# Kernel tuning notes

Hardware: AMD Instinct MI355X
Metric: run time of the kernel (lower is better)

The kernel has to match this reference:

```python
import jax, jax.numpy as jnp
import numpy as np
from math import sqrt as msqrt

D_MODEL, D_FF, N_HEADS, D_K, D_V = 1024, 4096, 16, 64, 64
NEG = -1e9

def gelu_erf(x):
    return 0.5 * x * (1.0 + jax.lax.erf(x / msqrt(2.0)))

def layer_norm(x, g, b, eps=1e-5):
    mu = jnp.mean(x, axis=-1, keepdims=True)
    var = jnp.mean(jnp.square(x - mu), axis=-1, keepdims=True)
    return (x - mu) * jax.lax.rsqrt(var + eps) * g + b

def setup_inputs() -> dict:
    key = jax.random.key(0)
    ks = jax.random.split(key, 12)
    B, S = 2, 2048
    s = lambda fan_in: 1.0 / msqrt(fan_in)
    inp = {
        "x": jax.random.normal(ks[0], (B, S, D_MODEL), dtype=jnp.float32),
        "pad_mask": jnp.zeros((B, S, S), dtype=bool),
        "W_Q": jax.random.uniform(ks[1], (D_MODEL, N_HEADS * D_K), minval=-s(D_MODEL), maxval=s(D_MODEL)),
        "W_K": jax.random.uniform(ks[2], (D_MODEL, N_HEADS * D_K), minval=-s(D_MODEL), maxval=s(D_MODEL)),
        "W_V": jax.random.uniform(ks[3], (D_MODEL, N_HEADS * D_V), minval=-s(D_MODEL), maxval=s(D_MODEL)),
        "W_O": jax.random.uniform(ks[4], (N_HEADS * D_V, D_MODEL), minval=-s(N_HEADS * D_V), maxval=s(N_HEADS * D_V)),
        "fc1_w": jax.random.uniform(ks[5], (D_MODEL, D_FF), minval=-s(D_MODEL), maxval=s(D_MODEL)),
        "fc1_b": jax.random.uniform(ks[6], (D_FF,), minval=-s(D_MODEL), maxval=s(D_MODEL)),
        "fc2_w": jax.random.uniform(ks[7], (D_FF, D_MODEL), minval=-s(D_FF), maxval=s(D_FF)),
        "fc2_b": jax.random.uniform(ks[8], (D_MODEL,), minval=-s(D_FF), maxval=s(D_FF)),
        "ln1_g": jnp.ones((D_MODEL,), jnp.float32),
        "ln1_b": jnp.zeros((D_MODEL,), jnp.float32),
        "ln2_g": jnp.ones((D_MODEL,), jnp.float32),
        "ln2_b": jnp.zeros((D_MODEL,), jnp.float32),
    }
    return inp

def reference(x, pad_mask, W_Q, W_K, W_V, W_O, fc1_w, fc1_b, fc2_w, fc2_b,
              ln1_g, ln1_b, ln2_g, ln2_b):
    B, S, _ = x.shape
    # --- pre-norm MHA ---
    residual = x
    h = layer_norm(x, ln1_g, ln1_b)
    q = (h @ W_Q).reshape(B, S, N_HEADS, D_K).transpose(0, 2, 1, 3)  # [B,H,S,dk]
    k = (h @ W_K).reshape(B, S, N_HEADS, D_K).transpose(0, 2, 1, 3)
    v = (h @ W_V).reshape(B, S, N_HEADS, D_V).transpose(0, 2, 1, 3)
    scores = jnp.einsum("bhqd,bhkd->bhqk", q, k) / msqrt(D_K)
    scores = jnp.where(pad_mask[:, None, :, :], NEG, scores)
    attn = jax.nn.softmax(scores, axis=-1)
    ctx = jnp.einsum("bhqk,bhkd->bhqd", attn, v)
    ctx = ctx.transpose(0, 2, 1, 3).reshape(B, S, N_HEADS * D_V)
    x = ctx @ W_O + residual
    # --- pre-norm FFN (dropout is identity at inference) ---
    residual = x
    h = layer_norm(x, ln2_g, ln2_b)
    h = gelu_erf(h @ fc1_w + fc1_b)
    x = h @ fc2_w + fc2_b + residual
    return x
```

## Files before the change

kernel.cpp:

```cpp
#include <hip/hip_runtime.h>
#include <hip/hip_bf16.h>
#include <math.h>

#define DI __device__ __forceinline__

typedef short s16x8 __attribute__((ext_vector_type(8)));
typedef unsigned short u16x8_t __attribute__((ext_vector_type(8)));
typedef float f32x4 __attribute__((ext_vector_type(4)));

static constexpr int T_TOK = 4096;
static constexpr int DM    = 1024;
static constexpr int DFF   = 4096;
static constexpr int S_LEN = 2048;
static constexpr int NB    = 2;
static constexpr int LDK   = 2048;

DI unsigned short f2bf(float f) {
    unsigned int u = __builtin_bit_cast(unsigned int, f);
    u += 0x7fffu + ((u >> 16) & 1u);
    return (unsigned short)(u >> 16);
}

DI unsigned pack_bf2(float a, float b) {
    unsigned ua = __builtin_bit_cast(unsigned, a) + 0x8000u;
    unsigned ub = __builtin_bit_cast(unsigned, b) + 0x8000u;
    return __builtin_amdgcn_perm(ub, ua, 0x07060302u);
}

DI float gelu_f(float x) {
    return 0.5f * x * (1.0f + erff(x * 0.70710678118654752440f));
}

DI int swz(int r) { return (r & 7) ^ ((r >> 3) & 7); }

DI void gload_lds16(const void* g, void* l) {
    __builtin_amdgcn_global_load_lds((const unsigned int*)g, (unsigned int*)l, 16, 0, 0);
}

__global__ __launch_bounds__(256) void tcvt_kernel(const float* __restrict__ in,
                                                   unsigned short* __restrict__ out,
                                                   int K, int N) {
    __shared__ float tile[32][33];
    const int tx = threadIdx.x & 31, ty = threadIdx.x >> 5;
    const int k0 = blockIdx.y * 32, n0 = blockIdx.x * 32;
#pragma unroll
    for (int i = 0; i < 4; ++i) {
        int k = ty + i * 8;
        tile[k][tx] = in[(size_t)(k0 + k) * N + n0 + tx];
    }
    __syncthreads();
#pragma unroll
    for (int i = 0; i < 4; ++i) {
        int n = ty + i * 8;
        out[(size_t)(n0 + n) * K + k0 + tx] = f2bf(tile[tx][n]);
    }
}

__global__ __launch_bounds__(256) void ln_kernel(const float* __restrict__ x,
                                                 const float* __restrict__ g,
                                                 const float* __restrict__ b,
                                                 unsigned short* __restrict__ out) {
    int row = blockIdx.x;
    int t = threadIdx.x;
    const float4 v = reinterpret_cast<const float4*>(x + (size_t)row * DM)[t];
    float s = v.x + v.y + v.z + v.w;
    float s2 = v.x * v.x + v.y * v.y + v.z * v.z + v.w * v.w;
#pragma unroll
    for (int m = 1; m < 64; m <<= 1) { s += __shfl_xor(s, m, 64); s2 += __shfl_xor(s2, m, 64); }
    __shared__ float red[8];
    int w = t >> 6;
    if ((t & 63) == 0) { red[w] = s; red[4 + w] = s2; }
    __syncthreads();
    s = red[0] + red[1] + red[2] + red[3];
    s2 = red[4] + red[5] + red[6] + red[7];
    float mu = s * (1.0f / DM);
    float var = s2 * (1.0f / DM) - mu * mu;
    float rs = rsqrtf(var + 1e-5f);
    float4 gv = reinterpret_cast<const float4*>(g)[t];
    float4 bv = reinterpret_cast<const float4*>(b)[t];
    ushort4 ov = make_ushort4(f2bf((v.x - mu) * rs * gv.x + bv.x),
                              f2bf((v.y - mu) * rs * gv.y + bv.y),
                              f2bf((v.z - mu) * rs * gv.z + bv.z),
                              f2bf((v.w - mu) * rs * gv.w + bv.w));
    reinterpret_cast<ushort4*>(out + (size_t)row * DM)[t] = ov;
}

template <int EPI, int BN>
__global__ __launch_bounds__(256) void gemm_kernel(const unsigned short* __restrict__ A,
                                                   const unsigned short* __restrict__ Bt,
                                                   const float* __restrict__ bias,
                                                   const float* __restrict__ resid,
                                                   void* __restrict__ Cv, void* __restrict__ Cv2,
                                                   int M, int N, int K) {
    constexpr int NN = BN / 32;
    constexpr int BCH = BN / 64;
    __shared__ unsigned short Asm[128][32];
    __shared__ unsigned short Bsm[BN][32];
    const int t = threadIdx.x, lane = t & 63, w = t >> 6;
    const int wr = w >> 1, wc = w & 1;
    const int m0 = blockIdx.y * 128, n0 = blockIdx.x * BN;
    const int c = lane & 15, g = lane >> 4;
    const int srow = lane >> 2, scol = (lane & 3) * 8;

    f32x4 acc[4][NN] = {};
    const unsigned short* Ab = A + (size_t)m0 * K;
    const unsigned short* Bb = Bt + (size_t)n0 * K;

    for (int k0 = 0; k0 < K; k0 += 32) {
        __syncthreads();
#pragma unroll
        for (int cc = 0; cc < 2; ++cc) {
            int ch = 2 * w + cc;
            int r = ch * 16 + srow;
            gload_lds16(Ab + (size_t)r * K + k0 + scol, &Asm[ch * 16][0]);
        }
#pragma unroll
        for (int cc = 0; cc < BCH; ++cc) {
            int ch = BCH * w + cc;
            int r = ch * 16 + srow;
            gload_lds16(Bb + (size_t)r * K + k0 + scol, &Bsm[ch * 16][0]);
        }
        __syncthreads();
        s16x8 af[4], bf[NN];
#pragma unroll
        for (int i = 0; i < 4; ++i)
            af[i] = *reinterpret_cast<const s16x8*>(&Asm[wr * 64 + i * 16 + c][g * 8]);
#pragma unroll
        for (int n = 0; n < NN; ++n)
            bf[n] = *reinterpret_cast<const s16x8*>(&Bsm[wc * (BN / 2) + n * 16 + c][g * 8]);
#pragma unroll
        for (int i = 0; i < 4; ++i)
#pragma unroll
            for (int n = 0; n < NN; ++n)
                acc[i][n] = __builtin_amdgcn_mfma_f32_16x16x32_bf16(af[i], bf[n], acc[i][n], 0, 0, 0);
    }

    const int crow = g * 4;
#pragma unroll
    for (int i = 0; i < 4; ++i) {
#pragma unroll
        for (int n = 0; n < NN; ++n) {
            const int col = n0 + wc * (BN / 2) + n * 16 + c;
#pragma unroll
            for (int j = 0; j < 4; ++j) {
                const int row = m0 + wr * 64 + i * 16 + crow + j;
                float v = acc[i][n][j];
                if constexpr (EPI == 2) {
                    v = gelu_f(v + bias[col]);
                    ((unsigned short*)Cv)[(size_t)row * N + col] = f2bf(v);
                } else if constexpr (EPI == 3) {
                    v = v + bias[col] + resid[(size_t)row * N + col];
                    ((float*)Cv)[(size_t)row * N + col] = v;
                } else if constexpr (EPI == 1) {
                    v = v + resid[(size_t)row * N + col];
                    ((float*)Cv)[(size_t)row * N + col] = v;
                } else {
                    if (col < 2048) {
                        float vv = (col < 1024) ? v * 0.125f : v;
                        ((unsigned short*)Cv)[(size_t)row * LDK + col] = f2bf(vv);
                    } else {
                        ((unsigned short*)Cv2)[(size_t)(col - 2048) * T_TOK + row] = f2bf(v);
                    }
                }
            }
        }
    }
}

__global__ __launch_bounds__(256) void attn_kernel(const unsigned short* __restrict__ QK,
                                                   const unsigned short* __restrict__ Vt,
                                                   const unsigned char* __restrict__ mask,
                                                   unsigned short* __restrict__ O) {
    const int qt = blockIdx.x, h = blockIdx.y, b = blockIdx.z;
    const int t = threadIdx.x, lane = t & 63, w = t >> 6;
    const int c = lane & 15, g = lane >> 4;
    const int crow = g * 4;
    const int qb0 = qt * 64;
    const int qw = qb0 + w * 16;
    const int swzc16 = swz(c) << 4;

    __shared__ unsigned short Ksm[2][64][64];
    __shared__ unsigned short Vsm[2][64][64];
    __shared__ unsigned short Psm[4][16][64];
    __shared__ unsigned char Msm[64][64];

    s16x8 qf[2];
    {
        const unsigned short* qp = QK + (size_t)(b * S_LEN + qw + c) * LDK + h * 64 + g * 8;
        qf[0] = *reinterpret_cast<const s16x8*>(qp);
        qf[1] = *reinterpret_cast<const s16x8*>(qp + 32);
    }

    float lsum = 0.f;
    f32x4 oacc[4] = {};

    const int vtok = t >> 2;
    const int vd0 = (t & 3) * 16;
    const unsigned char* mcol = mask + (size_t)b * S_LEN * S_LEN + (size_t)(qb0 + vtok) * S_LEN + vd0;
    const unsigned short* kg = QK + 1024;
    const int srow8 = lane >> 3, sslot = lane & 7;

    auto stage = [&](int buf, int kt) {
#pragma unroll
        for (int cc = 0; cc < 2; ++cc) {
            int ch = 2 * w + cc;
            int r = ch * 8 + srow8;
            int slot = sslot ^ swz(r);
            gload_lds16(kg + (size_t)(b * S_LEN + kt + r) * LDK + h * 64 + slot * 8,
                        &Ksm[buf][ch * 8][0]);
            gload_lds16(Vt + (size_t)(h * 64 + r) * T_TOK + b * S_LEN + kt + slot * 8,
                        &Vsm[buf][ch * 8][0]);
        }
    };

    stage(0, 0);
    uint4 mv0 = *reinterpret_cast<const uint4*>(mcol);
    asm volatile("s_waitcnt vmcnt(0)" ::: "memory");
    int anym = __syncthreads_or((mv0.x | mv0.y | mv0.z | mv0.w) != 0);
    if (anym) {
        *reinterpret_cast<uint4*>(&Msm[vtok][vd0]) = mv0;
        __syncthreads();
    }

    constexpr int NT = S_LEN / 64;
    for (int it = 0; it < NT; ++it) {
        const int cur = it & 1;
        uint4 mv = {0u, 0u, 0u, 0u};
        if (it < NT - 1) {
            stage(cur ^ 1, (it + 1) * 64);
            mv = *reinterpret_cast<const uint4*>(mcol + (it + 1) * 64);
        }

        f32x4 s[4] = {};
#pragma unroll
        for (int kh = 0; kh < 2; ++kh) {
#pragma unroll
            for (int kb = 0; kb < 4; ++kb) {
                int key = kb * 16 + c;
                int byte = key * 128 + (((kh * 4 + g) ^ swz(key)) << 4);
                s16x8 kf = *(const s16x8*)((const char*)&Ksm[cur][0][0] + byte);
                s[kb] = __builtin_amdgcn_mfma_f32_16x16x32_bf16(kf, qf[kh], s[kb], 0, 0, 0);
            }
        }
        if (anym) {
#pragma unroll
            for (int kb = 0; kb < 4; ++kb)
#pragma unroll
                for (int j = 0; j < 4; ++j)
                    if (Msm[w * 16 + c][kb * 16 + crow + j]) s[kb][j] = -1e9f;
        }

#pragma unroll
        for (int kb = 0; kb < 4; ++kb) {
            float p0 = __expf(s[kb][0]);
            float p1 = __expf(s[kb][1]);
            float p2 = __expf(s[kb][2]);
            float p3 = __expf(s[kb][3]);
            lsum += (p0 + p1) + (p2 + p3);
            uint2 pk = make_uint2(pack_bf2(p0, p1), pack_bf2(p2, p3));
            int byte = c * 128 + ((kb * 32 + g * 8) ^ swzc16);
            *(uint2*)((char*)&Psm[w][0][0] + byte) = pk;
        }

#pragma unroll
        for (int kh = 0; kh < 2; ++kh) {
            int pbyte = c * 128 + ((kh * 64 + g * 16) ^ swzc16);
            s16x8 pf = *(const s16x8*)((const char*)&Psm[w][0][0] + pbyte);
#pragma unroll
            for (int nb = 0; nb < 4; ++nb) {
                int d = nb * 16 + c;
                int byte = d * 128 + (((kh * 4 + g) ^ swz(d)) << 4);
                s16x8 vf = *(const s16x8*)((const char*)&Vsm[cur][0][0] + byte);
                oacc[nb] = __builtin_amdgcn_mfma_f32_16x16x32_bf16(pf, vf, oacc[nb], 0, 0, 0);
            }
        }

        asm volatile("s_waitcnt vmcnt(0)" ::: "memory");
        int nxt = __syncthreads_or((mv.x | mv.y | mv.z | mv.w) != 0);
        if (nxt) {
            *reinterpret_cast<uint4*>(&Msm[vtok][vd0]) = mv;
            __syncthreads();
        }
        anym = nxt;
    }

    lsum += __shfl_xor(lsum, 16);
    lsum += __shfl_xor(lsum, 32);
    float inv[4];
#pragma unroll
    for (int j = 0; j < 4; ++j) {
        float lq = __shfl(lsum, crow + j);
        inv[j] = lq > 0.f ? 1.0f / lq : 0.f;
    }
#pragma unroll
    for (int nb = 0; nb < 4; ++nb) {
#pragma unroll
        for (int j = 0; j < 4; ++j) {
            const size_t oo = (size_t)(b * S_LEN + qw + crow + j) * DM + h * 64 + nb * 16 + c;
            O[oo] = f2bf(oacc[nb][j] * inv[j]);
        }
    }
}

extern "C" void kernel_launch(void* const* d_in, const int* in_sizes, int n_in,
                              void* d_out, int out_size, void* d_ws, size_t ws_size,
                              hipStream_t stream) {
    (void)in_sizes; (void)n_in; (void)out_size; (void)ws_size;
    const float* x   = (const float*)d_in[0];
    const unsigned char* mask = (const unsigned char*)d_in[1];
    const float* WQ  = (const float*)d_in[2];
    const float* WK  = (const float*)d_in[3];
    const float* WV  = (const float*)d_in[4];
    const float* WO  = (const float*)d_in[5];
    const float* F1W = (const float*)d_in[6];
    const float* F1B = (const float*)d_in[7];
    const float* F2W = (const float*)d_in[8];
    const float* F2B = (const float*)d_in[9];
    const float* L1G = (const float*)d_in[10];
    const float* L1B = (const float*)d_in[11];
    const float* L2G = (const float*)d_in[12];
    const float* L2B = (const float*)d_in[13];
    float* out = (float*)d_out;

    char* ws = (char*)d_ws;
    size_t off = 0;
    auto alloc = [&](size_t bytes) -> void* {
        void* p = ws + off;
        off += (bytes + 255) & ~(size_t)255;
        return p;
    };
    unsigned short* h1    = (unsigned short*)alloc((size_t)T_TOK * DM * 2);
    unsigned short* qk    = (unsigned short*)alloc((size_t)T_TOK * LDK * 2);
    unsigned short* vt    = (unsigned short*)alloc((size_t)DM * T_TOK * 2);
    unsigned short* ctx   = (unsigned short*)alloc((size_t)T_TOK * DM * 2);
    float*          x2    = (float*)alloc((size_t)T_TOK * DM * 4);
    unsigned short* h2    = (unsigned short*)alloc((size_t)T_TOK * DM * 2);
    unsigned short* h3    = (unsigned short*)alloc((size_t)T_TOK * DFF * 2);
    unsigned short* WQKVt = (unsigned short*)alloc((size_t)3 * DM * DM * 2);
    unsigned short* WOt   = (unsigned short*)alloc((size_t)DM * DM * 2);
    unsigned short* F1Wt  = (unsigned short*)alloc((size_t)DFF * DM * 2);
    unsigned short* F2Wt  = (unsigned short*)alloc((size_t)DM * DFF * 2);

    dim3 t32(DM / 32, DM / 32);
    tcvt_kernel<<<t32, 256, 0, stream>>>(WQ, WQKVt, DM, DM);
    tcvt_kernel<<<t32, 256, 0, stream>>>(WK, WQKVt + (size_t)DM * DM, DM, DM);
    tcvt_kernel<<<t32, 256, 0, stream>>>(WV, WQKVt + (size_t)2 * DM * DM, DM, DM);
    tcvt_kernel<<<t32, 256, 0, stream>>>(WO, WOt, DM, DM);
    tcvt_kernel<<<dim3(DFF / 32, DM / 32), 256, 0, stream>>>(F1W, F1Wt, DM, DFF);
    tcvt_kernel<<<dim3(DM / 32, DFF / 32), 256, 0, stream>>>(F2W, F2Wt, DFF, DM);

    ln_kernel<<<T_TOK, 256, 0, stream>>>(x, L1G, L1B, h1);

    gemm_kernel<4, 128><<<dim3(3072 / 128, T_TOK / 128), 256, 0, stream>>>(
        h1, WQKVt, nullptr, nullptr, qk, vt, T_TOK, 3072, DM);

    attn_kernel<<<dim3(S_LEN / 64, 16, NB), 256, 0, stream>>>(qk, vt, mask, ctx);

    gemm_kernel<1, 64><<<dim3(DM / 64, T_TOK / 128), 256, 0, stream>>>(
        ctx, WOt, nullptr, x, x2, nullptr, T_TOK, DM, DM);

    ln_kernel<<<T_TOK, 256, 0, stream>>>(x2, L2G, L2B, h2);

    gemm_kernel<2, 128><<<dim3(DFF / 128, T_TOK / 128), 256, 0, stream>>>(
        h2, F1Wt, F1B, nullptr, h3, nullptr, T_TOK, DFF, DM);
    gemm_kernel<3, 64><<<dim3(DM / 64, T_TOK / 128), 256, 0, stream>>>(
        h3, F2Wt, F2B, x2, out, nullptr, T_TOK, DM, DFF);
}
```

Baseline: 475.2 us.

## Triple-buffer GEMM LDS tiles and overlap global loads with MFMA compute

Turns the GEMM main loop from a load-sync-compute-sync pattern into a three-stage software pipeline over LDS buffers. Two k-tiles are prefetched ahead, explicit vmcnt waits let the next tile's loads stay in flight, and one barrier per iteration replaces two. The aim is to hide global-to-LDS load latency behind MFMA work. The cost is triple the LDS footprint per block, which may lower occupancy, and reliance on hand-counted vmcnt values tied to how many loads each stage issues.

```diff
diff --git a/kernel.cpp b/kernel.cpp
--- a/kernel.cpp
+++ b/kernel.cpp
@@ -94,8 +94,8 @@
                                                    int M, int N, int K) {
     constexpr int NN = BN / 32;
     constexpr int BCH = BN / 64;
-    __shared__ unsigned short Asm[128][32];
-    __shared__ unsigned short Bsm[BN][32];
+    __shared__ unsigned short Asm[3][128][32];
+    __shared__ unsigned short Bsm[3][BN][32];
     const int t = threadIdx.x, lane = t & 63, w = t >> 6;
     const int wr = w >> 1, wc = w & 1;
     const int m0 = blockIdx.y * 128, n0 = blockIdx.x * BN;
@@ -106,34 +106,54 @@
     const unsigned short* Ab = A + (size_t)m0 * K;
     const unsigned short* Bb = Bt + (size_t)n0 * K;
 
-    for (int k0 = 0; k0 < K; k0 += 32) {
-        __syncthreads();
+    auto stage = [&](int buf, int k0) {
 #pragma unroll
         for (int cc = 0; cc < 2; ++cc) {
             int ch = 2 * w + cc;
             int r = ch * 16 + srow;
-            gload_lds16(Ab + (size_t)r * K + k0 + scol, &Asm[ch * 16][0]);
+            gload_lds16(Ab + (size_t)r * K + k0 + scol, &Asm[buf][ch * 16][0]);
         }
 #pragma unroll
         for (int cc = 0; cc < BCH; ++cc) {
             int ch = BCH * w + cc;
             int r = ch * 16 + srow;
-            gload_lds16(Bb + (size_t)r * K + k0 + scol, &Bsm[ch * 16][0]);
-        }
-        __syncthreads();
+            gload_lds16(Bb + (size_t)r * K + k0 + scol, &Bsm[buf][ch * 16][0]);
+        }
+    };
+
+    auto compute = [&](int buf) {
         s16x8 af[4], bf[NN];
 #pragma unroll
         for (int i = 0; i < 4; ++i)
-            af[i] = *reinterpret_cast<const s16x8*>(&Asm[wr * 64 + i * 16 + c][g * 8]);
+            af[i] = *reinterpret_cast<const s16x8*>(&Asm[buf][wr * 64 + i * 16 + c][g * 8]);
 #pragma unroll
         for (int n = 0; n < NN; ++n)
-            bf[n] = *reinterpret_cast<const s16x8*>(&Bsm[wc * (BN / 2) + n * 16 + c][g * 8]);
+            bf[n] = *reinterpret_cast<const s16x8*>(&Bsm[buf][wc * (BN / 2) + n * 16 + c][g * 8]);
 #pragma unroll
         for (int i = 0; i < 4; ++i)
 #pragma unroll
             for (int n = 0; n < NN; ++n)
                 acc[i][n] = __builtin_amdgcn_mfma_f32_16x16x32_bf16(af[i], bf[n], acc[i][n], 0, 0, 0);
-    }
+    };
+
+    const int NK = K >> 5;
+    stage(0, 0);
+    stage(1, 32);
+    int buf = 0;
+    for (int i = 0; i < NK - 1; ++i) {
+        if constexpr (BCH == 2) asm volatile("s_waitcnt vmcnt(4)" ::: "memory");
+        else                    asm volatile("s_waitcnt vmcnt(3)" ::: "memory");
+        __builtin_amdgcn_s_barrier();
+        compute(buf);
+        if (i + 2 < NK) {
+            int nb = buf + 2; if (nb >= 3) nb -= 3;
+            stage(nb, (i + 2) << 5);
+        }
+        ++buf; if (buf == 3) buf = 0;
+    }
+    asm volatile("s_waitcnt vmcnt(0)" ::: "memory");
+    __builtin_amdgcn_s_barrier();
+    compute(buf);
 
     const int crow = g * 4;
 #pragma unroll
```

After: 457.1 us. 1.04x faster.
